# Performance work log

Hardware: AMD Instinct MI355X
Metric: run time of the kernel (lower is better)

Reference implementation:

```python
import jax, jax.numpy as jnp
import numpy as np
import math

# tcnn HashGrid config (hard-coded in the torch module)
N_LEVELS = 16
N_FEATS = 2
LOG2_T = 19
T = 1 << LOG2_T            # 524288 entries per level
BASE_RES = 16
PER_LEVEL_SCALE = 1.4472692012786865
PRIMES = (1, 2654435761, 805459861)  # tcnn coherent spatial hash primes
N_POINTS = 1 << 20

# 8 trilinear corner offsets, [8, 3]
_OFFSETS = np.stack(np.meshgrid(*([np.arange(2)] * 3), indexing='ij'), -1).reshape(8, 3)


def _level_scale_res(level):
    # tcnn: grid_scale = base * s^l - 1 ; resolution = ceil(grid_scale) + 1
    scale = BASE_RES * (PER_LEVEL_SCALE ** level) - 1.0
    res = int(math.ceil(scale)) + 1
    return scale, res


def hashgrid_encode(coords, table):
    """coords: [..., 3] in [0,1]; table: [N_LEVELS, T, N_FEATS].
    Returns [..., N_LEVELS * N_FEATS]."""
    lead_shape = coords.shape[:-1]
    x = coords.reshape(-1, 3)                         # [N, 3]
    offs_i = jnp.asarray(_OFFSETS, dtype=jnp.uint32)  # [8, 3]
    offs_f = jnp.asarray(_OFFSETS, dtype=coords.dtype)
    feats = []
    for l in range(N_LEVELS):
        scale, res = _level_scale_res(l)
        pos = x * jnp.asarray(scale, x.dtype) + 0.5   # [N, 3]
        pf = jnp.floor(pos)
        w = pos - pf                                   # trilinear weights in [0,1)
        grid = pf.astype(jnp.uint32)                  # [N, 3]
        c = grid[None, :, :] + offs_i[:, None, :]     # [8, N, 3] corner coords
        if res ** 3 <= T:
            # dense (non-hashed) indexing for coarse levels
            cc = jnp.minimum(c, jnp.uint32(res - 1)).astype(jnp.int32)
            idx = cc[..., 0] + cc[..., 1] * res + cc[..., 2] * (res * res)
        else:
            # spatial hash: XOR of per-dim prime products, mod 2^19
            h = (c[..., 0] * jnp.uint32(PRIMES[0])
                 ^ c[..., 1] * jnp.uint32(PRIMES[1])
                 ^ c[..., 2] * jnp.uint32(PRIMES[2]))
            idx = (h & jnp.uint32(T - 1)).astype(jnp.int32)
        v = table[l][idx]                             # [8, N, F] gathered features
        # per-corner trilinear weight: prod over dims of (w or 1-w)
        wc = jnp.prod(jnp.where(offs_f[:, None, :] == 1.0, w[None], 1.0 - w[None]), axis=-1)  # [8, N]
        feats.append(jnp.einsum('kn,knf->nf', wc, v))  # [N, F]
    out = jnp.concatenate(feats, axis=-1)             # [N, 32]
    return out.reshape(*lead_shape, N_LEVELS * N_FEATS)


def setup_inputs() -> dict:
    key = jax.random.key(0)
    k1, k2 = jax.random.split(key)
    coords = jax.random.uniform(k1, (N_POINTS, 3), dtype=jnp.float32)
    # tcnn initializes hash table uniform in [-1e-4, 1e-4]
    table = jax.random.uniform(k2, (N_LEVELS, T, N_FEATS), dtype=jnp.float32,
                               minval=-1e-4, maxval=1e-4)
    return {"coords": coords, "table": table}


def reference(coords, table):
    return hashgrid_encode(coords, table)
```

## Files before the change

### kernel.cpp

```cpp
#include <hip/hip_runtime.h>
#include <math.h>

#define TBL   (1u << 19)
#define TMASK (TBL - 1u)
#define PRIME1 2654435761u
#define PRIME2 805459861u

typedef float v2f __attribute__((ext_vector_type(2)));
typedef float v4f __attribute__((ext_vector_type(4)));

struct LevelParams {
    float    scale[16];
    unsigned res[16];
    unsigned dense[16];
};

__device__ __forceinline__ void corner_indices(
    float x, float y, float z, float s, unsigned res, unsigned dense,
    unsigned idx[8], float* wx, float* wy, float* wz)
{
    float px = __fadd_rn(__fmul_rn(x, s), 0.5f);
    float py = __fadd_rn(__fmul_rn(y, s), 0.5f);
    float pz = __fadd_rn(__fmul_rn(z, s), 0.5f);
    float fx = floorf(px), fy = floorf(py), fz = floorf(pz);
    *wx = px - fx; *wy = py - fy; *wz = pz - fz;
    unsigned gx = (unsigned)fx, gy = (unsigned)fy, gz = (unsigned)fz;

    if (dense) {
        const unsigned rm1 = res - 1u;
        unsigned cx0 = min(gx, rm1),   cx1 = min(gx + 1u, rm1);
        unsigned cy0 = min(gy, rm1),   cy1 = min(gy + 1u, rm1);
        unsigned cz0 = min(gz, rm1),   cz1 = min(gz + 1u, rm1);
        unsigned y0 = cy0 * res,       y1 = cy1 * res;
        unsigned z0 = cz0 * res * res, z1 = cz1 * res * res;
        idx[0] = cx0 + y0 + z0;  idx[1] = cx0 + y0 + z1;
        idx[2] = cx0 + y1 + z0;  idx[3] = cx0 + y1 + z1;
        idx[4] = cx1 + y0 + z0;  idx[5] = cx1 + y0 + z1;
        idx[6] = cx1 + y1 + z0;  idx[7] = cx1 + y1 + z1;
    } else {
        unsigned hx0 = gx,          hx1 = gx + 1u;
        unsigned hy0 = gy * PRIME1, hy1 = hy0 + PRIME1;
        unsigned hz0 = gz * PRIME2, hz1 = hz0 + PRIME2;
        idx[0] = (hx0 ^ hy0 ^ hz0) & TMASK;
        idx[1] = (hx0 ^ hy0 ^ hz1) & TMASK;
        idx[2] = (hx0 ^ hy1 ^ hz0) & TMASK;
        idx[3] = (hx0 ^ hy1 ^ hz1) & TMASK;
        idx[4] = (hx1 ^ hy0 ^ hz0) & TMASK;
        idx[5] = (hx1 ^ hy0 ^ hz1) & TMASK;
        idx[6] = (hx1 ^ hy1 ^ hz0) & TMASK;
        idx[7] = (hx1 ^ hy1 ^ hz1) & TMASK;
    }
}

__device__ __forceinline__ v2f interp_level(
    const v4f* __restrict__ tab4,
    float x, float y, float z, float s, unsigned res, unsigned dense)
{
    unsigned idx[8];
    float wx, wy, wz;
    corner_indices(x, y, z, s, res, dense, idx, &wx, &wy, &wz);

    float wx0 = 1.f - wx, wy0 = 1.f - wy, wz0 = 1.f - wz;
    float wyz00 = wy0 * wz0, wyz01 = wy0 * wz;
    float wyz10 = wy  * wz0, wyz11 = wy  * wz;
    float cw0[4] = { wx0 * wyz00, wx0 * wyz01, wx0 * wyz10, wx0 * wyz11 };
    float cw1[4] = { wx  * wyz00, wx  * wyz01, wx  * wyz10, wx  * wyz11 };

    float f0 = 0.f, f1 = 0.f;
    #pragma unroll
    for (int k = 0; k < 4; ++k) {
        unsigned i0 = idx[k], i1 = idx[k + 4];
        v4f q0 = tab4[i0 >> 1];
        v4f q1 = tab4[i1 >> 1];
        float a0 = (i0 & 1u) ? q0.z : q0.x;
        float b0 = (i0 & 1u) ? q0.w : q0.y;
        float a1 = (i1 & 1u) ? q1.z : q1.x;
        float b1 = (i1 & 1u) ? q1.w : q1.y;
        f0 = fmaf(cw0[k], a0, f0);
        f1 = fmaf(cw0[k], b0, f1);
        f0 = fmaf(cw1[k], a1, f0);
        f1 = fmaf(cw1[k], b1, f1);
    }
    v2f r; r.x = f0; r.y = f1;
    return r;
}

__global__ __launch_bounds__(256, 8) void pass_a(
    const float* __restrict__ coords,
    const float* __restrict__ table,
    v2f* __restrict__ ws,
    LevelParams lp, unsigned n)
{
    const unsigned l = blockIdx.y;
    const unsigned p = blockIdx.x * 256u + threadIdx.x;
    if (p >= n) return;

    const float x = coords[3ull * p + 0];
    const float y = coords[3ull * p + 1];
    const float z = coords[3ull * p + 2];

    const v4f* __restrict__ tab4 = (const v4f*)(table + (size_t)l * (2u * TBL));
    v2f r = interp_level(tab4, x, y, z, lp.scale[l], lp.res[l], lp.dense[l]);
    __builtin_nontemporal_store(r, ws + (size_t)l * n + p);
}

__global__ __launch_bounds__(256, 8) void pass_b(
    const v2f* __restrict__ ws,
    float* __restrict__ out, unsigned n)
{
    const unsigned p = blockIdx.x * 256u + threadIdx.x;
    if (p >= n) return;

    v2f v[16];
    #pragma unroll
    for (int l = 0; l < 16; ++l)
        v[l] = ws[(size_t)l * n + p];

    v4f* __restrict__ out4 = (v4f*)out;
    #pragma unroll
    for (int i = 0; i < 8; ++i) {
        v4f o;
        o.x = v[2 * i].x;     o.y = v[2 * i].y;
        o.z = v[2 * i + 1].x; o.w = v[2 * i + 1].y;
        out4[(size_t)p * 8u + i] = o;
    }
}

__global__ __launch_bounds__(256, 4) void hashgrid_enc(
    const float* __restrict__ coords,
    const float* __restrict__ table,
    float* __restrict__ out,
    LevelParams lp, unsigned n)
{
    __shared__ float lds[256 * 33];
    const unsigned t = threadIdx.x;
    const unsigned p = blockIdx.x * 256u + t;

    float x = 0.f, y = 0.f, z = 0.f;
    if (p < n) {
        x = coords[3ull * p + 0];
        y = coords[3ull * p + 1];
        z = coords[3ull * p + 2];
    }

    #pragma unroll 2
    for (int l = 0; l < 16; ++l) {
        const v4f* __restrict__ tab4 = (const v4f*)(table + (size_t)l * (2u * TBL));
        v2f r = interp_level(tab4, x, y, z, lp.scale[l], lp.res[l], lp.dense[l]);
        lds[t * 33u + 2u * l]      = r.x;
        lds[t * 33u + 2u * l + 1u] = r.y;
    }
    __syncthreads();

    const size_t base  = (size_t)blockIdx.x * 8192u;
    const size_t total = (size_t)n * 32u;
    #pragma unroll
    for (int i = 0; i < 32; ++i) {
        size_t j = (size_t)i * 256u + t;
        size_t o = base + j;
        if (o < total)
            out[o] = lds[(unsigned)(j >> 5) * 33u + ((unsigned)j & 31u)];
    }
}

extern "C" void kernel_launch(void* const* d_in, const int* in_sizes, int n_in,
                              void* d_out, int out_size, void* d_ws, size_t ws_size,
                              hipStream_t stream) {
    (void)n_in; (void)out_size;
    const float* coords = (const float*)d_in[0];
    const float* table  = (const float*)d_in[1];
    float* out = (float*)d_out;

    LevelParams lp;
    for (int l = 0; l < 16; ++l) {
        double scale = 16.0 * pow(1.4472692012786865, (double)l) - 1.0;
        int res = (int)ceil(scale) + 1;
        lp.scale[l] = (float)scale;
        lp.res[l]   = (unsigned)res;
        long long r3 = (long long)res * res * res;
        lp.dense[l] = (r3 <= (long long)TBL) ? 1u : 0u;
    }

    unsigned n = (unsigned)(in_sizes[0] / 3);
    unsigned chunks = (n + 255u) / 256u;
    size_t ws_needed = (size_t)16 * n * sizeof(v2f);

    if (ws_size >= ws_needed) {
        v2f* ws = (v2f*)d_ws;
        hipLaunchKernelGGL(pass_a, dim3(chunks, 16), dim3(256), 0, stream,
                           coords, table, ws, lp, n);
        hipLaunchKernelGGL(pass_b, dim3(chunks), dim3(256), 0, stream,
                           ws, out, n);
    } else {
        hipLaunchKernelGGL(hashgrid_enc, dim3(chunks), dim3(256), 0, stream,
                           coords, table, out, lp, n);
    }
}
```

Measured before the change: 691.9 us.

## Compute dense levels in the gather/transpose pass, write only hashed levels to workspace

Pass A now handles only the 11 hashed levels, whose workspace footprint shrinks accordingly. The 5 dense, cache-friendly levels are computed directly in pass B, which then transposes through LDS and emits coalesced nontemporal vector stores. This cuts workspace write and read traffic and removes 5/16 of pass A's blocks. The cost is more work and a lower occupancy bound in pass B. It also hard-codes that levels 0-4 are dense, which holds for this config.

After: 662.6 us. 4.2% less time.

```diff
diff --git a/kernel.cpp b/kernel.cpp
--- a/kernel.cpp
+++ b/kernel.cpp
@@ -5,6 +5,9 @@
 #define TMASK (TBL - 1u)
 #define PRIME1 2654435761u
 #define PRIME2 805459861u
+
+#define N_DENSE  5u
+#define N_HASH   11u
 
 typedef float v2f __attribute__((ext_vector_type(2)));
 typedef float v4f __attribute__((ext_vector_type(4)));
@@ -91,8 +94,9 @@
     v2f* __restrict__ ws,
     LevelParams lp, unsigned n)
 {
-    const unsigned l = blockIdx.y;
-    const unsigned p = blockIdx.x * 256u + threadIdx.x;
+    const unsigned li = blockIdx.y;
+    const unsigned l  = li + N_DENSE;
+    const unsigned p  = blockIdx.x * 256u + threadIdx.x;
     if (p >= n) return;
 
     const float x = coords[3ull * p + 0];
@@ -100,29 +104,66 @@
     const float z = coords[3ull * p + 2];
 
     const v4f* __restrict__ tab4 = (const v4f*)(table + (size_t)l * (2u * TBL));
-    v2f r = interp_level(tab4, x, y, z, lp.scale[l], lp.res[l], lp.dense[l]);
-    __builtin_nontemporal_store(r, ws + (size_t)l * n + p);
-}
-
-__global__ __launch_bounds__(256, 8) void pass_b(
+    v2f r = interp_level(tab4, x, y, z, lp.scale[l], lp.res[l], 0u);
+    ws[(size_t)li * n + p] = r;
+}
+
+__global__ __launch_bounds__(256, 4) void pass_b(
+    const float* __restrict__ coords,
+    const float* __restrict__ table,
     const v2f* __restrict__ ws,
-    float* __restrict__ out, unsigned n)
-{
-    const unsigned p = blockIdx.x * 256u + threadIdx.x;
-    if (p >= n) return;
-
-    v2f v[16];
-    #pragma unroll
-    for (int l = 0; l < 16; ++l)
-        v[l] = ws[(size_t)l * n + p];
+    float* __restrict__ out,
+    LevelParams lp, unsigned n)
+{
+    __shared__ float lds[256 * 33];
+    const unsigned t  = threadIdx.x;
+    const unsigned p0 = blockIdx.x * 256u;
+    const unsigned p  = p0 + t;
+
+    float x = 0.f, y = 0.f, z = 0.f;
+    if (p < n) {
+        x = coords[3ull * p + 0];
+        y = coords[3ull * p + 1];
+        z = coords[3ull * p + 2];
+    }
+
+    #pragma unroll
+    for (int l = 0; l < (int)N_DENSE; ++l) {
+        v2f r = {0.f, 0.f};
+        if (p < n) {
+            const v4f* __restrict__ tab4 =
+                (const v4f*)(table + (size_t)l * (2u * TBL));
+            r = interp_level(tab4, x, y, z, lp.scale[l], lp.res[l], 1u);
+        }
+        lds[t * 33u + 2u * l]      = r.x;
+        lds[t * 33u + 2u * l + 1u] = r.y;
+    }
+
+    #pragma unroll
+    for (int l = 0; l < (int)N_HASH; ++l) {
+        v2f v = {0.f, 0.f};
+        if (p < n) v = ws[(size_t)l * n + p];
+        lds[t * 33u + 2u * (l + N_DENSE)]      = v.x;
+        lds[t * 33u + 2u * (l + N_DENSE) + 1u] = v.y;
+    }
+    __syncthreads();
 
     v4f* __restrict__ out4 = (v4f*)out;
+    const size_t base4  = (size_t)p0 * 8u;
+    const size_t total4 = (size_t)n * 8u;
     #pragma unroll
     for (int i = 0; i < 8; ++i) {
-        v4f o;
-        o.x = v[2 * i].x;     o.y = v[2 * i].y;
-        o.z = v[2 * i + 1].x; o.w = v[2 * i + 1].y;
-        out4[(size_t)p * 8u + i] = o;
+        unsigned j = (unsigned)i * 256u + t;
+        size_t o = base4 + j;
+        if (o < total4) {
+            unsigned pt = j >> 3, c = (j & 7u) * 4u;
+            v4f q;
+            q.x = lds[pt * 33u + c + 0u];
+            q.y = lds[pt * 33u + c + 1u];
+            q.z = lds[pt * 33u + c + 2u];
+            q.w = lds[pt * 33u + c + 3u];
+            __builtin_nontemporal_store(q, out4 + o);
+        }
     }
 }
 
@@ -183,14 +224,14 @@
 
     unsigned n = (unsigned)(in_sizes[0] / 3);
     unsigned chunks = (n + 255u) / 256u;
-    size_t ws_needed = (size_t)16 * n * sizeof(v2f);
+    size_t ws_needed = (size_t)N_HASH * n * sizeof(v2f);
 
     if (ws_size >= ws_needed) {
         v2f* ws = (v2f*)d_ws;
-        hipLaunchKernelGGL(pass_a, dim3(chunks, 16), dim3(256), 0, stream,
+        hipLaunchKernelGGL(pass_a, dim3(chunks, N_HASH), dim3(256), 0, stream,
                            coords, table, ws, lp, n);
         hipLaunchKernelGGL(pass_b, dim3(chunks), dim3(256), 0, stream,
-                           ws, out, n);
+                           coords, table, ws, out, lp, n);
     } else {
         hipLaunchKernelGGL(hashgrid_enc, dim3(chunks), dim3(256), 0, stream,
                            coords, table, out, lp, n);
```

## Replace two-pass workspace scheme with single fused per-point kernel and vectorized stores

Applied to the files above, without the earlier changes.

Drops the level-major pass_a plus transpose pass_b path that went through a workspace, and always runs the fused kernel that loops over all 16 levels per point, stages results in LDS and writes output. The output write now uses 16-byte nontemporal vector stores instead of scalar stores. This removes the 128 MB workspace round trip and a second launch. In exchange, each block now gathers across all 16 tables, which loses the per-level locality of table accesses in L2 that the level-major grid provided.

Result: slower. 852.9 us (+23.3%).

```diff
diff --git a/kernel.cpp b/kernel.cpp
--- a/kernel.cpp
+++ b/kernel.cpp
@@ -85,56 +85,16 @@
     return r;
 }
 
-__global__ __launch_bounds__(256, 8) void pass_a(
-    const float* __restrict__ coords,
-    const float* __restrict__ table,
-    v2f* __restrict__ ws,
-    LevelParams lp, unsigned n)
-{
-    const unsigned l = blockIdx.y;
-    const unsigned p = blockIdx.x * 256u + threadIdx.x;
-    if (p >= n) return;
-
-    const float x = coords[3ull * p + 0];
-    const float y = coords[3ull * p + 1];
-    const float z = coords[3ull * p + 2];
-
-    const v4f* __restrict__ tab4 = (const v4f*)(table + (size_t)l * (2u * TBL));
-    v2f r = interp_level(tab4, x, y, z, lp.scale[l], lp.res[l], lp.dense[l]);
-    __builtin_nontemporal_store(r, ws + (size_t)l * n + p);
-}
-
-__global__ __launch_bounds__(256, 8) void pass_b(
-    const v2f* __restrict__ ws,
-    float* __restrict__ out, unsigned n)
-{
-    const unsigned p = blockIdx.x * 256u + threadIdx.x;
-    if (p >= n) return;
-
-    v2f v[16];
-    #pragma unroll
-    for (int l = 0; l < 16; ++l)
-        v[l] = ws[(size_t)l * n + p];
-
-    v4f* __restrict__ out4 = (v4f*)out;
-    #pragma unroll
-    for (int i = 0; i < 8; ++i) {
-        v4f o;
-        o.x = v[2 * i].x;     o.y = v[2 * i].y;
-        o.z = v[2 * i + 1].x; o.w = v[2 * i + 1].y;
-        out4[(size_t)p * 8u + i] = o;
-    }
-}
-
-__global__ __launch_bounds__(256, 4) void hashgrid_enc(
+__global__ __launch_bounds__(256, 4) void fused_enc(
     const float* __restrict__ coords,
     const float* __restrict__ table,
     float* __restrict__ out,
     LevelParams lp, unsigned n)
 {
     __shared__ float lds[256 * 33];
-    const unsigned t = threadIdx.x;
-    const unsigned p = blockIdx.x * 256u + t;
+    const unsigned t  = threadIdx.x;
+    const unsigned p0 = blockIdx.x * 256u;
+    const unsigned p  = p0 + t;
 
     float x = 0.f, y = 0.f, z = 0.f;
     if (p < n) {
@@ -145,28 +105,38 @@
 
     #pragma unroll 2
     for (int l = 0; l < 16; ++l) {
-        const v4f* __restrict__ tab4 = (const v4f*)(table + (size_t)l * (2u * TBL));
-        v2f r = interp_level(tab4, x, y, z, lp.scale[l], lp.res[l], lp.dense[l]);
+        const v4f* __restrict__ tab4 =
+            (const v4f*)(table + (size_t)l * (2u * TBL));
+        v2f r = interp_level(tab4, x, y, z, lp.scale[l], lp.res[l],
+                             lp.dense[l]);
         lds[t * 33u + 2u * l]      = r.x;
         lds[t * 33u + 2u * l + 1u] = r.y;
     }
     __syncthreads();
 
-    const size_t base  = (size_t)blockIdx.x * 8192u;
-    const size_t total = (size_t)n * 32u;
+    v4f* __restrict__ out4 = (v4f*)out;
+    const size_t base4  = (size_t)p0 * 8u;
+    const size_t total4 = (size_t)n * 8u;
     #pragma unroll
-    for (int i = 0; i < 32; ++i) {
-        size_t j = (size_t)i * 256u + t;
-        size_t o = base + j;
-        if (o < total)
-            out[o] = lds[(unsigned)(j >> 5) * 33u + ((unsigned)j & 31u)];
+    for (int i = 0; i < 8; ++i) {
+        unsigned j = (unsigned)i * 256u + t;
+        size_t o = base4 + j;
+        if (o < total4) {
+            unsigned pt = j >> 3, c = (j & 7u) * 4u;
+            v4f q;
+            q.x = lds[pt * 33u + c + 0u];
+            q.y = lds[pt * 33u + c + 1u];
+            q.z = lds[pt * 33u + c + 2u];
+            q.w = lds[pt * 33u + c + 3u];
+            __builtin_nontemporal_store(q, out4 + o);
+        }
     }
 }
 
 extern "C" void kernel_launch(void* const* d_in, const int* in_sizes, int n_in,
                               void* d_out, int out_size, void* d_ws, size_t ws_size,
                               hipStream_t stream) {
-    (void)n_in; (void)out_size;
+    (void)n_in; (void)out_size; (void)d_ws; (void)ws_size;
     const float* coords = (const float*)d_in[0];
     const float* table  = (const float*)d_in[1];
     float* out = (float*)d_out;
@@ -183,16 +153,7 @@
 
     unsigned n = (unsigned)(in_sizes[0] / 3);
     unsigned chunks = (n + 255u) / 256u;
-    size_t ws_needed = (size_t)16 * n * sizeof(v2f);
 
-    if (ws_size >= ws_needed) {
-        v2f* ws = (v2f*)d_ws;
-        hipLaunchKernelGGL(pass_a, dim3(chunks, 16), dim3(256), 0, stream,
-                           coords, table, ws, lp, n);
-        hipLaunchKernelGGL(pass_b, dim3(chunks), dim3(256), 0, stream,
-                           ws, out, n);
-    } else {
-        hipLaunchKernelGGL(hashgrid_enc, dim3(chunks), dim3(256), 0, stream,
-                           coords, table, out, lp, n);
-    }
+    hipLaunchKernelGGL(fused_enc, dim3(chunks), dim3(256), 0, stream,
+                       coords, table, out, lp, n);
 }
```

## Share one 16-byte load for even-x hashed corner pairs; LDS-transpose output pass

Applied to the files above, without the earlier changes.

For hashed levels, when gx is even, the x0 and x1 corners differ only in the lowest index bit. Both therefore sit in the same 16-byte entry pair, so one v4f load serves both corners and halves table gathers for about half the points. pass_b now reads two points per thread with 16-byte loads, transposes through padded LDS, and writes fully coalesced nontemporal 16-byte stores instead of strided per-thread stores. The price is divergence between the even and odd branches, extra LDS traffic and syncs, and lower occupancy bounds in pass_b.

Measured after the change: 630.3 us. 8.9% less time.

```diff
diff --git a/kernel.cpp b/kernel.cpp
--- a/kernel.cpp
+++ b/kernel.cpp
@@ -15,71 +15,111 @@
     unsigned dense[16];
 };
 
-__device__ __forceinline__ void corner_indices(
-    float x, float y, float z, float s, unsigned res, unsigned dense,
-    unsigned idx[8], float* wx, float* wy, float* wz)
+__device__ __forceinline__ void split_pos(
+    float x, float y, float z, float s,
+    unsigned* gx, unsigned* gy, unsigned* gz,
+    float* wx, float* wy, float* wz)
 {
     float px = __fadd_rn(__fmul_rn(x, s), 0.5f);
     float py = __fadd_rn(__fmul_rn(y, s), 0.5f);
     float pz = __fadd_rn(__fmul_rn(z, s), 0.5f);
     float fx = floorf(px), fy = floorf(py), fz = floorf(pz);
     *wx = px - fx; *wy = py - fy; *wz = pz - fz;
-    unsigned gx = (unsigned)fx, gy = (unsigned)fy, gz = (unsigned)fz;
-
-    if (dense) {
-        const unsigned rm1 = res - 1u;
-        unsigned cx0 = min(gx, rm1),   cx1 = min(gx + 1u, rm1);
-        unsigned cy0 = min(gy, rm1),   cy1 = min(gy + 1u, rm1);
-        unsigned cz0 = min(gz, rm1),   cz1 = min(gz + 1u, rm1);
-        unsigned y0 = cy0 * res,       y1 = cy1 * res;
-        unsigned z0 = cz0 * res * res, z1 = cz1 * res * res;
-        idx[0] = cx0 + y0 + z0;  idx[1] = cx0 + y0 + z1;
-        idx[2] = cx0 + y1 + z0;  idx[3] = cx0 + y1 + z1;
-        idx[4] = cx1 + y0 + z0;  idx[5] = cx1 + y0 + z1;
-        idx[6] = cx1 + y1 + z0;  idx[7] = cx1 + y1 + z1;
-    } else {
-        unsigned hx0 = gx,          hx1 = gx + 1u;
-        unsigned hy0 = gy * PRIME1, hy1 = hy0 + PRIME1;
-        unsigned hz0 = gz * PRIME2, hz1 = hz0 + PRIME2;
-        idx[0] = (hx0 ^ hy0 ^ hz0) & TMASK;
-        idx[1] = (hx0 ^ hy0 ^ hz1) & TMASK;
-        idx[2] = (hx0 ^ hy1 ^ hz0) & TMASK;
-        idx[3] = (hx0 ^ hy1 ^ hz1) & TMASK;
-        idx[4] = (hx1 ^ hy0 ^ hz0) & TMASK;
-        idx[5] = (hx1 ^ hy0 ^ hz1) & TMASK;
-        idx[6] = (hx1 ^ hy1 ^ hz0) & TMASK;
-        idx[7] = (hx1 ^ hy1 ^ hz1) & TMASK;
-    }
-}
-
-__device__ __forceinline__ v2f interp_level(
-    const v4f* __restrict__ tab4,
-    float x, float y, float z, float s, unsigned res, unsigned dense)
-{
-    unsigned idx[8];
-    float wx, wy, wz;
-    corner_indices(x, y, z, s, res, dense, idx, &wx, &wy, &wz);
-
+    *gx = (unsigned)fx; *gy = (unsigned)fy; *gz = (unsigned)fz;
+}
+
+__device__ __forceinline__ void corner_w(
+    float wx, float wy, float wz, float cw0[4], float cw1[4])
+{
     float wx0 = 1.f - wx, wy0 = 1.f - wy, wz0 = 1.f - wz;
     float wyz00 = wy0 * wz0, wyz01 = wy0 * wz;
     float wyz10 = wy  * wz0, wyz11 = wy  * wz;
-    float cw0[4] = { wx0 * wyz00, wx0 * wyz01, wx0 * wyz10, wx0 * wyz11 };
-    float cw1[4] = { wx  * wyz00, wx  * wyz01, wx  * wyz10, wx  * wyz11 };
-
+    cw0[0] = wx0 * wyz00; cw0[1] = wx0 * wyz01;
+    cw0[2] = wx0 * wyz10; cw0[3] = wx0 * wyz11;
+    cw1[0] = wx  * wyz00; cw1[1] = wx  * wyz01;
+    cw1[2] = wx  * wyz10; cw1[3] = wx  * wyz11;
+}
+
+__device__ __forceinline__ v2f interp_dense(
+    const v4f* __restrict__ tab4,
+    float x, float y, float z, float s, unsigned res)
+{
+    unsigned gx, gy, gz; float wx, wy, wz;
+    split_pos(x, y, z, s, &gx, &gy, &gz, &wx, &wy, &wz);
+    const unsigned rm1 = res - 1u;
+    unsigned cx0 = min(gx, rm1),   cx1 = min(gx + 1u, rm1);
+    unsigned cy0 = min(gy, rm1),   cy1 = min(gy + 1u, rm1);
+    unsigned cz0 = min(gz, rm1),   cz1 = min(gz + 1u, rm1);
+    unsigned y0 = cy0 * res,       y1 = cy1 * res;
+    unsigned z0 = cz0 * res * res, z1 = cz1 * res * res;
+    unsigned i0[4] = { cx0+y0+z0, cx0+y0+z1, cx0+y1+z0, cx0+y1+z1 };
+    unsigned i1[4] = { cx1+y0+z0, cx1+y0+z1, cx1+y1+z0, cx1+y1+z1 };
+
+    float cw0[4], cw1[4];
+    corner_w(wx, wy, wz, cw0, cw1);
     float f0 = 0.f, f1 = 0.f;
     #pragma unroll
     for (int k = 0; k < 4; ++k) {
-        unsigned i0 = idx[k], i1 = idx[k + 4];
-        v4f q0 = tab4[i0 >> 1];
-        v4f q1 = tab4[i1 >> 1];
-        float a0 = (i0 & 1u) ? q0.z : q0.x;
-        float b0 = (i0 & 1u) ? q0.w : q0.y;
-        float a1 = (i1 & 1u) ? q1.z : q1.x;
-        float b1 = (i1 & 1u) ? q1.w : q1.y;
+        v4f q0 = tab4[i0[k] >> 1];
+        v4f q1 = tab4[i1[k] >> 1];
+        float a0 = (i0[k] & 1u) ? q0.z : q0.x;
+        float b0 = (i0[k] & 1u) ? q0.w : q0.y;
+        float a1 = (i1[k] & 1u) ? q1.z : q1.x;
+        float b1 = (i1[k] & 1u) ? q1.w : q1.y;
         f0 = fmaf(cw0[k], a0, f0);
         f1 = fmaf(cw0[k], b0, f1);
         f0 = fmaf(cw1[k], a1, f0);
         f1 = fmaf(cw1[k], b1, f1);
+    }
+    v2f r; r.x = f0; r.y = f1;
+    return r;
+}
+
+__device__ __forceinline__ v2f interp_hashed(
+    const v4f* __restrict__ tab4,
+    float x, float y, float z, float s)
+{
+    unsigned gx, gy, gz; float wx, wy, wz;
+    split_pos(x, y, z, s, &gx, &gy, &gz, &wx, &wy, &wz);
+    unsigned hy0 = gy * PRIME1, hy1 = hy0 + PRIME1;
+    unsigned hz0 = gz * PRIME2, hz1 = hz0 + PRIME2;
+    unsigned b0[4] = { (gx^hy0^hz0)&TMASK, (gx^hy0^hz1)&TMASK,
+                       (gx^hy1^hz0)&TMASK, (gx^hy1^hz1)&TMASK };
+
+    float cw0[4], cw1[4];
+    corner_w(wx, wy, wz, cw0, cw1);
+    float f0 = 0.f, f1 = 0.f;
+
+    if ((gx & 1u) == 0u) {
+        #pragma unroll
+        for (int k = 0; k < 4; ++k) {
+            unsigned i0 = b0[k];
+            v4f q = tab4[i0 >> 1];
+            bool odd = (i0 & 1u) != 0u;
+            float a0 = odd ? q.z : q.x, c0 = odd ? q.w : q.y;
+            float a1 = odd ? q.x : q.z, c1 = odd ? q.y : q.w;
+            f0 = fmaf(cw0[k], a0, f0);
+            f1 = fmaf(cw0[k], c0, f1);
+            f0 = fmaf(cw1[k], a1, f0);
+            f1 = fmaf(cw1[k], c1, f1);
+        }
+    } else {
+        unsigned gx1 = gx + 1u;
+        unsigned b1[4] = { (gx1^hy0^hz0)&TMASK, (gx1^hy0^hz1)&TMASK,
+                           (gx1^hy1^hz0)&TMASK, (gx1^hy1^hz1)&TMASK };
+        #pragma unroll
+        for (int k = 0; k < 4; ++k) {
+            v4f q0 = tab4[b0[k] >> 1];
+            v4f q1 = tab4[b1[k] >> 1];
+            float a0 = (b0[k] & 1u) ? q0.z : q0.x;
+            float c0 = (b0[k] & 1u) ? q0.w : q0.y;
+            float a1 = (b1[k] & 1u) ? q1.z : q1.x;
+            float c1 = (b1[k] & 1u) ? q1.w : q1.y;
+            f0 = fmaf(cw0[k], a0, f0);
+            f1 = fmaf(cw0[k], c0, f1);
+            f0 = fmaf(cw1[k], a1, f0);
+            f1 = fmaf(cw1[k], c1, f1);
+        }
     }
     v2f r; r.x = f0; r.y = f1;
     return r;
@@ -100,29 +140,66 @@
     const float z = coords[3ull * p + 2];
 
     const v4f* __restrict__ tab4 = (const v4f*)(table + (size_t)l * (2u * TBL));
-    v2f r = interp_level(tab4, x, y, z, lp.scale[l], lp.res[l], lp.dense[l]);
+    v2f r = lp.dense[l]
+        ? interp_dense (tab4, x, y, z, lp.scale[l], lp.res[l])
+        : interp_hashed(tab4, x, y, z, lp.scale[l]);
     __builtin_nontemporal_store(r, ws + (size_t)l * n + p);
 }
 
-__global__ __launch_bounds__(256, 8) void pass_b(
+__global__ __launch_bounds__(256, 4) void pass_b(
     const v2f* __restrict__ ws,
     float* __restrict__ out, unsigned n)
 {
-    const unsigned p = blockIdx.x * 256u + threadIdx.x;
-    if (p >= n) return;
-
-    v2f v[16];
-    #pragma unroll
-    for (int l = 0; l < 16; ++l)
-        v[l] = ws[(size_t)l * n + p];
+    __shared__ float lds[256 * 33];
+    const unsigned t  = threadIdx.x;
+    const unsigned p0 = blockIdx.x * 512u;
+    const unsigned pb = p0 + 2u * t;
+
+    v4f v[16];
+    #pragma unroll
+    for (int l = 0; l < 16; ++l) {
+        v4f q = {0.f, 0.f, 0.f, 0.f};
+        if (pb + 1u < n) {
+            q = *(const v4f*)(ws + (size_t)l * n + pb);
+        } else if (pb < n) {
+            v2f h = ws[(size_t)l * n + pb];
+            q.x = h.x; q.y = h.y;
+        }
+        v[l] = q;
+    }
 
     v4f* __restrict__ out4 = (v4f*)out;
-    #pragma unroll
-    for (int i = 0; i < 8; ++i) {
-        v4f o;
-        o.x = v[2 * i].x;     o.y = v[2 * i].y;
-        o.z = v[2 * i + 1].x; o.w = v[2 * i + 1].y;
-        out4[(size_t)p * 8u + i] = o;
+    const size_t total4 = (size_t)n * 8u;
+
+    #pragma unroll
+    for (int r = 0; r < 2; ++r) {
+        __syncthreads();
+        if ((t >> 7) == (unsigned)r) {
+            const unsigned lp0 = 2u * (t & 127u);
+            #pragma unroll
+            for (int l = 0; l < 16; ++l) {
+                lds[lp0 * 33u + 2u * l]            = v[l].x;
+                lds[lp0 * 33u + 2u * l + 1u]       = v[l].y;
+                lds[(lp0 + 1u) * 33u + 2u * l]     = v[l].z;
+                lds[(lp0 + 1u) * 33u + 2u * l + 1u]= v[l].w;
+            }
+        }
+        __syncthreads();
+        const unsigned pr0 = p0 + 256u * (unsigned)r;
+        #pragma unroll
+        for (int i = 0; i < 8; ++i) {
+            unsigned j  = (unsigned)i * 256u + t;
+            unsigned pt = j >> 3, c = (j & 7u);
+            size_t o = (size_t)(pr0 + pt) * 8u + c;
+            if (o < total4) {
+                v4f q;
+                q.x = lds[pt * 33u + c * 4u + 0u];
+                q.y = lds[pt * 33u + c * 4u + 1u];
+                q.z = lds[pt * 33u + c * 4u + 2u];
+                q.w = lds[pt * 33u + c * 4u + 3u];
+                __builtin_nontemporal_store(q, out4 + o);
+            }
+        }
     }
 }
 
@@ -146,7 +223,9 @@
     #pragma unroll 2
     for (int l = 0; l < 16; ++l) {
         const v4f* __restrict__ tab4 = (const v4f*)(table + (size_t)l * (2u * TBL));
-        v2f r = interp_level(tab4, x, y, z, lp.scale[l], lp.res[l], lp.dense[l]);
+        v2f r = lp.dense[l]
+            ? interp_dense (tab4, x, y, z, lp.scale[l], lp.res[l])
+            : interp_hashed(tab4, x, y, z, lp.scale[l]);
         lds[t * 33u + 2u * l]      = r.x;
         lds[t * 33u + 2u * l + 1u] = r.y;
     }
@@ -189,7 +268,8 @@
         v2f* ws = (v2f*)d_ws;
         hipLaunchKernelGGL(pass_a, dim3(chunks, 16), dim3(256), 0, stream,
                            coords, table, ws, lp, n);
-        hipLaunchKernelGGL(pass_b, dim3(chunks), dim3(256), 0, stream,
+        unsigned chunks_b = (n + 511u) / 512u;
+        hipLaunchKernelGGL(pass_b, dim3(chunks_b), dim3(256), 0, stream,
                            ws, out, n);
     } else {
         hipLaunchKernelGGL(hashgrid_enc, dim3(chunks), dim3(256), 0, stream,
```
